# Kernel tuning notes

Measured on AMD Instinct MI355X. Metric: run time of the kernel, lower is better.

## Reference

```python
import jax, jax.numpy as jnp
import numpy as np

D_MODEL = 1024
N_Q = 16
N_KV = 4
HEAD = 64
T = 4096
B = 1


def setup_inputs() -> dict:
    key = jax.random.key(0)
    ks = jax.random.split(key, 5)
    q_dim = N_Q * HEAD
    kv_dim = N_KV * HEAD
    s = 0.02
    return {
        "x": jax.random.normal(ks[0], (B, T, D_MODEL), dtype=jnp.float32),
        "W_q": jax.random.normal(ks[1], (D_MODEL, q_dim), dtype=jnp.float32) * s,
        "W_k": jax.random.normal(ks[2], (D_MODEL, kv_dim), dtype=jnp.float32) * s,
        "W_v": jax.random.normal(ks[3], (D_MODEL, kv_dim), dtype=jnp.float32) * s,
        "W_o": jax.random.normal(ks[4], (q_dim, D_MODEL), dtype=jnp.float32) * s,
    }


def reference(x, W_q, W_k, W_v, W_o):
    Bsz, Tlen, _ = x.shape
    n_q_per_kv = N_Q // N_KV
    scale = jnp.asarray(np.sqrt(HEAD), x.dtype)
    # projections, split heads: (B, T, H*D) -> (B, H, T, D)
    q = (x @ W_q).reshape(Bsz, Tlen, N_Q, HEAD).transpose(0, 2, 1, 3)
    k = (x @ W_k).reshape(Bsz, Tlen, N_KV, HEAD).transpose(0, 2, 1, 3)
    v = (x @ W_v).reshape(Bsz, Tlen, N_KV, HEAD).transpose(0, 2, 1, 3)
    # GQA: duplicate KV heads to match query heads (repeat_interleave on head dim)
    k = jnp.repeat(k, n_q_per_kv, axis=1)
    v = jnp.repeat(v, n_q_per_kv, axis=1)
    attn = jnp.einsum("bhqd,bhkd->bhqk", q, k) / scale  # (B, H, T, T)
    causal = jnp.tril(jnp.ones((Tlen, Tlen), dtype=bool))
    attn = jnp.where(causal[None, None], attn, -jnp.inf)
    attn = jax.nn.softmax(attn, axis=-1)
    out = jnp.einsum("bhqk,bhkd->bhqd", attn, v)  # (B, H, T, D)
    out = out.transpose(0, 2, 1, 3).reshape(Bsz, Tlen, N_Q * HEAD)
    return out @ W_o
```

## Files before the change

### kernel.cpp

```cpp
#include <hip/hip_runtime.h>

typedef __bf16 bf16;
typedef __bf16 bf16x4 __attribute__((ext_vector_type(4)));
typedef __bf16 bf16x8 __attribute__((ext_vector_type(8)));
typedef float  f32x4  __attribute__((ext_vector_type(4)));

#define DEV __device__ __forceinline__

#if __has_builtin(__builtin_amdgcn_exp2f)
#define EXP2(x) __builtin_amdgcn_exp2f(x)
#else
#define EXP2(x) exp2f(x)
#endif

DEV void gload16(const void* g, void* l) {
  __builtin_amdgcn_global_load_lds((const __attribute__((address_space(1))) void*)g,
                                   (__attribute__((address_space(3))) void*)l, 16, 0, 0);
}

DEV f32x4 mfma16(bf16x8 a, bf16x8 b, f32x4 c) {
  return __builtin_amdgcn_mfma_f32_16x16x32_bf16(a, b, c, 0, 0, 0);
}

#define QSCALE 0.18033688011112042f

__global__ __launch_bounds__(256) void cast_x_kernel(const float* __restrict__ x,
                                                     bf16* __restrict__ xb) {
  int i = blockIdx.x * 256 + threadIdx.x;
  f32x4 v = ((const f32x4*)x)[i];
  bf16x4 o = {(bf16)v.x, (bf16)v.y, (bf16)v.z, (bf16)v.w};
  ((bf16x4*)xb)[i] = o;
}

__global__ __launch_bounds__(256) void wtrans_kernel(const float* __restrict__ sQ,
                                                     const float* __restrict__ sK,
                                                     const float* __restrict__ sV,
                                                     bf16* __restrict__ dst) {
  __shared__ float tile[32][33];
  int k0 = blockIdx.x * 32, n0 = blockIdx.y * 32;
  int tx = threadIdx.x & 31, ty = threadIdx.x >> 5;
  const float* src; int ld, nb;
  if (n0 < 1024)      { src = sQ; ld = 1024; nb = 0; }
  else if (n0 < 1280) { src = sK; ld = 256;  nb = 1024; }
  else                { src = sV; ld = 256;  nb = 1280; }
#pragma unroll
  for (int i = 0; i < 4; i++) {
    int r = ty + 8 * i;
    tile[r][tx] = src[(size_t)(k0 + r) * ld + (n0 - nb + tx)];
  }
  __syncthreads();
#pragma unroll
  for (int i = 0; i < 4; i++) {
    int r = ty + 8 * i;
    dst[(size_t)(n0 + r) * 1024 + k0 + tx] = (bf16)tile[tx][r];
  }
}

template <int MODE>
__global__ __launch_bounds__(256) void gemm_kernel(const bf16* __restrict__ A,
                                                   const bf16* __restrict__ B,
                                                   float* __restrict__ Cf,
                                                   bf16* __restrict__ qkbuf,
                                                   bf16* __restrict__ vtbuf, int N) {
  constexpr int K = 1024;
  __shared__ bf16 Al[2][64 * 32];
  __shared__ bf16 Bl[2][128 * 32];
  int tid = threadIdx.x;
  int w = tid >> 6, lane = tid & 63;
  int g = lane >> 4, r15 = lane & 15;
  int wr = w >> 1, wc = w & 1;
  int m0 = blockIdx.y * 64, n0 = blockIdx.x * 128;

  int sra = 16 * w + (lane >> 2);
  int srb = 32 * w + (lane >> 2);
  int ss = lane & 3;
  const bf16* a0 = A + (size_t)(m0 + sra) * K + 8 * (ss ^ ((sra >> 1) & 3));
  const bf16* b0 = B + (size_t)(n0 + srb) * K + 8 * (ss ^ ((srb >> 1) & 3));
  const bf16* b1 = B + (size_t)(n0 + srb + 16) * K + 8 * (ss ^ (((srb + 16) >> 1) & 3));

#define GSTAGE(kk_, b_) do { \
    char* ad = (char*)Al[b_] + w * 1024; \
    char* bd = (char*)Bl[b_] + w * 2048; \
    gload16(a0 + (kk_), ad); \
    gload16(b0 + (kk_), bd); \
    gload16(b1 + (kk_), bd + 1024); \
  } while (0)

  GSTAGE(0, 0);
  __syncthreads();

  f32x4 acc[2][4] = {};
  for (int kk = 0; kk < K; kk += 32) {
    int cur = (kk >> 5) & 1;
    if (kk + 32 < K) GSTAGE(kk + 32, cur ^ 1);
    bf16x8 af[2], bb[4];
#pragma unroll
    for (int i = 0; i < 2; i++) {
      int m = 32 * wr + 16 * i + r15;
      af[i] = *(const bf16x8*)((const char*)Al[cur] + m * 64 + 16 * (g ^ ((m >> 1) & 3)));
    }
#pragma unroll
    for (int i = 0; i < 4; i++) {
      int n = 64 * wc + 16 * i + r15;
      bb[i] = *(const bf16x8*)((const char*)Bl[cur] + n * 64 + 16 * (g ^ ((n >> 1) & 3)));
    }
    __builtin_amdgcn_s_setprio(1);
#pragma unroll
    for (int mi = 0; mi < 2; mi++)
#pragma unroll
      for (int ni = 0; ni < 4; ni++)
        acc[mi][ni] = mfma16(af[mi], bb[ni], acc[mi][ni]);
    __builtin_amdgcn_s_setprio(0);
    __syncthreads();
  }

  if (MODE == 0) {
#pragma unroll
    for (int mi = 0; mi < 2; mi++) {
      int mg = m0 + 32 * wr + 16 * mi + 4 * g;
#pragma unroll
      for (int ni = 0; ni < 4; ni++) {
        int ng = n0 + 64 * wc + 16 * ni + r15;
#pragma unroll
        for (int r = 0; r < 4; r++)
          Cf[(size_t)(mg + r) * N + ng] = acc[mi][ni][r];
      }
    }
  } else {
    if (n0 < 1280) {
      float qs = (n0 < 1024) ? QSCALE : 1.0f;
#pragma unroll
      for (int mi = 0; mi < 2; mi++) {
        int tg = m0 + 32 * wr + 16 * mi + 4 * g;
#pragma unroll
        for (int ni = 0; ni < 4; ni++) {
          int ng = n0 + 64 * wc + 16 * ni + r15;
#pragma unroll
          for (int r = 0; r < 4; r++)
            qkbuf[(size_t)(tg + r) * 1280 + ng] = (bf16)(acc[mi][ni][r] * qs);
        }
      }
    } else {
#pragma unroll
      for (int mi = 0; mi < 2; mi++) {
        int tg = m0 + 32 * wr + 16 * mi + 4 * g;
#pragma unroll
        for (int ni = 0; ni < 4; ni++) {
          int vcol = n0 + 64 * wc + 16 * ni + r15 - 1280;
          bf16x4 pk = {(bf16)acc[mi][ni][0], (bf16)acc[mi][ni][1],
                       (bf16)acc[mi][ni][2], (bf16)acc[mi][ni][3]};
          *(bf16x4*)(vtbuf + (size_t)vcol * 4096 + tg) = pk;
        }
      }
    }
  }
#undef GSTAGE
}

__global__ __launch_bounds__(256) void attn_kernel(const bf16* __restrict__ qk,
                                                   const bf16* __restrict__ vt,
                                                   bf16* __restrict__ out) {
  __shared__ bf16 Kt[2][64 * 64];
  __shared__ bf16 Vt[2][64 * 64];
  __shared__ bf16 Pl[4][16][72];
  int tid = threadIdx.x, w = tid >> 6, lane = tid & 63;
  int g = lane >> 4, r15 = lane & 15;
  int j = blockIdx.x;
  int h = j & 15, tI = 63 - (j >> 4);
  int kh = h >> 2;
  int na = tI + 1;
  int qw = 64 * tI + 16 * w;

  bf16x8 bq[2];
#pragma unroll
  for (int ks = 0; ks < 2; ks++)
    bq[ks] = *(const bf16x8*)(qk + (size_t)(qw + r15) * 1280 + h * 64 + 32 * ks + 8 * g);

  float l_run = 0.f;
  f32x4 oacc[4] = {};

  int sw8 = 8 * ((lane & 7) ^ (lane >> 3));
  const bf16* kbase = qk + 1024 + (size_t)kh * 64 + (size_t)(16 * w + (lane >> 3)) * 1280 + sw8;
  const bf16* vbase = vt + ((size_t)(kh * 64 + 16 * w + (lane >> 3))) * 4096 + sw8;

#define STAGE(t0_, b_) do { \
    char* kd = (char*)Kt[b_] + w * 2048; \
    char* vd = (char*)Vt[b_] + w * 2048; \
    gload16(kbase + (size_t)(t0_) * 1280, kd); \
    gload16(kbase + (size_t)(t0_) * 1280 + (size_t)8 * 1280, kd + 1024); \
    gload16(vbase + (t0_), vd); \
    gload16(vbase + (t0_) + 8 * 4096, vd + 1024); \
  } while (0)

  STAGE(0, 0);
  __syncthreads();

  for (int it = 0; it < na; ++it) {
    int cur = it & 1;
    int t0 = 64 * it;
    if (it + 1 < na) STAGE(64 * (it + 1), cur ^ 1);
    bool need_mask = (it == na - 1);
    const char* Kc = (const char*)Kt[cur];
    const char* Vc = (const char*)Vt[cur];

    f32x4 s[4];
    __builtin_amdgcn_s_setprio(1);
#pragma unroll
    for (int mi = 0; mi < 4; mi++) {
      int kv = 16 * mi + r15;
      bf16x8 k0f = *(const bf16x8*)(Kc + kv * 128 + 16 * (g ^ (kv & 7)));
      bf16x8 k1f = *(const bf16x8*)(Kc + kv * 128 + 16 * ((4 + g) ^ (kv & 7)));
      f32x4 z = {};
      z = mfma16(k0f, bq[0], z);
      z = mfma16(k1f, bq[1], z);
      s[mi] = z;
    }
    __builtin_amdgcn_s_setprio(0);

    int qg = qw + r15;
    float psum = 0.f;
    bf16 pb[16];
#pragma unroll
    for (int mi = 0; mi < 4; mi++)
#pragma unroll
      for (int r = 0; r < 4; r++) {
        float v = s[mi][r];
        if (need_mask) {
          int kvg = t0 + 16 * mi + 4 * g + r;
          v = (kvg > qg) ? -1e30f : v;
        }
        float pp = EXP2(v);
        psum += pp;
        pb[4 * mi + r] = (bf16)pp;
      }
    l_run += psum;

#pragma unroll
    for (int mi = 0; mi < 4; mi++) {
      bf16x4 pk = {pb[4 * mi], pb[4 * mi + 1], pb[4 * mi + 2], pb[4 * mi + 3]};
      *(bf16x4*)((char*)&Pl[w][r15][0] + mi * 32 + g * 8) = pk;
    }
    bf16x8 ap0 = *(const bf16x8*)((const char*)&Pl[w][r15][0] + 16 * g);
    bf16x8 ap1 = *(const bf16x8*)((const char*)&Pl[w][r15][0] + 64 + 16 * g);
    __builtin_amdgcn_s_setprio(1);
#pragma unroll
    for (int ni = 0; ni < 4; ni++) {
      int d = 16 * ni + r15;
      bf16x8 bv0 = *(const bf16x8*)(Vc + d * 128 + 16 * (g ^ (d & 7)));
      bf16x8 bv1 = *(const bf16x8*)(Vc + d * 128 + 16 * ((4 + g) ^ (d & 7)));
      oacc[ni] = mfma16(ap0, bv0, oacc[ni]);
      oacc[ni] = mfma16(ap1, bv1, oacc[ni]);
    }
    __builtin_amdgcn_s_setprio(0);
    __syncthreads();
  }
#undef STAGE

  float lsum = l_run;
  lsum += __shfl_xor(lsum, 16);
  lsum += __shfl_xor(lsum, 32);
  float linv = 1.0f / lsum;
  float li[4];
#pragma unroll
  for (int r = 0; r < 4; r++) li[r] = __shfl(linv, 4 * g + r);
#pragma unroll
  for (int ni = 0; ni < 4; ni++)
#pragma unroll
    for (int r = 0; r < 4; r++)
      out[(size_t)(qw + 4 * g + r) * 1024 + h * 64 + 16 * ni + r15] =
          (bf16)(oacc[ni][r] * li[r]);
}

extern "C" void kernel_launch(void* const* d_in, const int* in_sizes, int n_in,
                              void* d_out, int out_size, void* d_ws, size_t ws_size,
                              hipStream_t stream) {
  const float* x  = (const float*)d_in[0];
  const float* Wq = (const float*)d_in[1];
  const float* Wk = (const float*)d_in[2];
  const float* Wv = (const float*)d_in[3];
  const float* Wo = (const float*)d_in[4];
  float* out = (float*)d_out;
  char* ws = (char*)d_ws;
  bf16* xb    = (bf16*)(ws);
  bf16* wqkvt = (bf16*)(ws + 8388608);
  bf16* wot   = (bf16*)(ws + 11534336);
  bf16* qkbuf = (bf16*)(ws + 13631488);
  bf16* vtb   = (bf16*)(ws + 24117248);

  cast_x_kernel<<<4096, 256, 0, stream>>>(x, xb);
  wtrans_kernel<<<dim3(32, 48), 256, 0, stream>>>(Wq, Wk, Wv, wqkvt);
  wtrans_kernel<<<dim3(32, 32), 256, 0, stream>>>(Wo, Wo, Wo, wot);
  gemm_kernel<1><<<dim3(12, 64), 256, 0, stream>>>(xb, wqkvt, nullptr, qkbuf, vtb, 1536);
  attn_kernel<<<dim3(1024), 256, 0, stream>>>(qkbuf, vtb, xb);
  gemm_kernel<0><<<dim3(8, 64), 256, 0, stream>>>(xb, wot, out, nullptr, nullptr, 1024);
}
```

Measured before the change: 184.5 us.

## Merge prep kernels into one launch and double GEMM K-tile to 64

Combines the x cast and the two weight transpose/cast kernels into a single prep kernel that dispatches on block index, removing two kernel launches. The GEMM now stages 64-wide K slices per iteration instead of 32, with a new 8-way XOR swizzle for 128-byte LDS rows, which halves the number of barriers and loop iterations. The cost is double the LDS footprint per block (48KB instead of 24KB), which may reduce occupancy, and more registers held for fragments.

```diff
diff --git a/kernel.cpp b/kernel.cpp
--- a/kernel.cpp
+++ b/kernel.cpp
@@ -24,25 +24,35 @@
 
 #define QSCALE 0.18033688011112042f
 
-__global__ __launch_bounds__(256) void cast_x_kernel(const float* __restrict__ x,
-                                                     bf16* __restrict__ xb) {
-  int i = blockIdx.x * 256 + threadIdx.x;
-  f32x4 v = ((const f32x4*)x)[i];
-  bf16x4 o = {(bf16)v.x, (bf16)v.y, (bf16)v.z, (bf16)v.w};
-  ((bf16x4*)xb)[i] = o;
-}
-
-__global__ __launch_bounds__(256) void wtrans_kernel(const float* __restrict__ sQ,
-                                                     const float* __restrict__ sK,
-                                                     const float* __restrict__ sV,
-                                                     bf16* __restrict__ dst) {
+__global__ __launch_bounds__(256) void prep_kernel(const float* __restrict__ x,
+                                                   const float* __restrict__ Wq,
+                                                   const float* __restrict__ Wk,
+                                                   const float* __restrict__ Wv,
+                                                   const float* __restrict__ Wo,
+                                                   bf16* __restrict__ xb,
+                                                   bf16* __restrict__ wqkvt,
+                                                   bf16* __restrict__ wot) {
   __shared__ float tile[32][33];
-  int k0 = blockIdx.x * 32, n0 = blockIdx.y * 32;
+  int bid = blockIdx.x;
+  if (bid < 4096) {
+    int i = bid * 256 + threadIdx.x;
+    f32x4 v = ((const f32x4*)x)[i];
+    bf16x4 o = {(bf16)v.x, (bf16)v.y, (bf16)v.z, (bf16)v.w};
+    ((bf16x4*)xb)[i] = o;
+    return;
+  }
+  const float* src; int ld, nb; bf16* dst; int idx;
+  if (bid < 5632) {
+    idx = bid - 4096; dst = wqkvt;
+    int n0 = (idx >> 5) * 32;
+    if (n0 < 1024)      { src = Wq; ld = 1024; nb = 0; }
+    else if (n0 < 1280) { src = Wk; ld = 256;  nb = 1024; }
+    else                { src = Wv; ld = 256;  nb = 1280; }
+  } else {
+    idx = bid - 5632; dst = wot; src = Wo; ld = 1024; nb = 0;
+  }
+  int k0 = (idx & 31) * 32, n0 = (idx >> 5) * 32;
   int tx = threadIdx.x & 31, ty = threadIdx.x >> 5;
-  const float* src; int ld, nb;
-  if (n0 < 1024)      { src = sQ; ld = 1024; nb = 0; }
-  else if (n0 < 1280) { src = sK; ld = 256;  nb = 1024; }
-  else                { src = sV; ld = 256;  nb = 1280; }
 #pragma unroll
   for (int i = 0; i < 4; i++) {
     int r = ty + 8 * i;
@@ -63,53 +73,64 @@
                                                    bf16* __restrict__ qkbuf,
                                                    bf16* __restrict__ vtbuf, int N) {
   constexpr int K = 1024;
-  __shared__ bf16 Al[2][64 * 32];
-  __shared__ bf16 Bl[2][128 * 32];
+  __shared__ bf16 Al[2][64 * 64];
+  __shared__ bf16 Bl[2][128 * 64];
   int tid = threadIdx.x;
   int w = tid >> 6, lane = tid & 63;
   int g = lane >> 4, r15 = lane & 15;
   int wr = w >> 1, wc = w & 1;
   int m0 = blockIdx.y * 64, n0 = blockIdx.x * 128;
 
-  int sra = 16 * w + (lane >> 2);
-  int srb = 32 * w + (lane >> 2);
-  int ss = lane & 3;
-  const bf16* a0 = A + (size_t)(m0 + sra) * K + 8 * (ss ^ ((sra >> 1) & 3));
-  const bf16* b0 = B + (size_t)(n0 + srb) * K + 8 * (ss ^ ((srb >> 1) & 3));
-  const bf16* b1 = B + (size_t)(n0 + srb + 16) * K + 8 * (ss ^ (((srb + 16) >> 1) & 3));
+  int sl = lane & 7;
+  int srw = lane >> 3;
+  const bf16* Abase = A + (size_t)m0 * K;
+  const bf16* Bbase = B + (size_t)n0 * K;
 
 #define GSTAGE(kk_, b_) do { \
-    char* ad = (char*)Al[b_] + w * 1024; \
-    char* bd = (char*)Bl[b_] + w * 2048; \
-    gload16(a0 + (kk_), ad); \
-    gload16(b0 + (kk_), bd); \
-    gload16(b1 + (kk_), bd + 1024); \
+    _Pragma("unroll") \
+    for (int i = 0; i < 2; i++) { \
+      int ra = 16 * w + 8 * i + srw; \
+      gload16(Abase + (size_t)ra * K + (kk_) + 8 * (sl ^ (ra & 7)), \
+              (char*)Al[b_] + (16 * w + 8 * i) * 128); \
+    } \
+    _Pragma("unroll") \
+    for (int i = 0; i < 4; i++) { \
+      int rb = 32 * w + 8 * i + srw; \
+      gload16(Bbase + (size_t)rb * K + (kk_) + 8 * (sl ^ (rb & 7)), \
+              (char*)Bl[b_] + (32 * w + 8 * i) * 128); \
+    } \
   } while (0)
 
   GSTAGE(0, 0);
   __syncthreads();
 
   f32x4 acc[2][4] = {};
-  for (int kk = 0; kk < K; kk += 32) {
-    int cur = (kk >> 5) & 1;
-    if (kk + 32 < K) GSTAGE(kk + 32, cur ^ 1);
-    bf16x8 af[2], bb[4];
-#pragma unroll
-    for (int i = 0; i < 2; i++) {
-      int m = 32 * wr + 16 * i + r15;
-      af[i] = *(const bf16x8*)((const char*)Al[cur] + m * 64 + 16 * (g ^ ((m >> 1) & 3)));
-    }
-#pragma unroll
-    for (int i = 0; i < 4; i++) {
-      int n = 64 * wc + 16 * i + r15;
-      bb[i] = *(const bf16x8*)((const char*)Bl[cur] + n * 64 + 16 * (g ^ ((n >> 1) & 3)));
+  for (int kk = 0; kk < K; kk += 64) {
+    int cur = (kk >> 6) & 1;
+    if (kk + 64 < K) GSTAGE(kk + 64, cur ^ 1);
+    bf16x8 af[2][2], bb[4][2];
+#pragma unroll
+    for (int mi = 0; mi < 2; mi++) {
+      int m = 32 * wr + 16 * mi + r15;
+#pragma unroll
+      for (int ks = 0; ks < 2; ks++)
+        af[mi][ks] = *(const bf16x8*)((const char*)Al[cur] + m * 128 + 16 * ((4 * ks + g) ^ (m & 7)));
+    }
+#pragma unroll
+    for (int ni = 0; ni < 4; ni++) {
+      int n = 64 * wc + 16 * ni + r15;
+#pragma unroll
+      for (int ks = 0; ks < 2; ks++)
+        bb[ni][ks] = *(const bf16x8*)((const char*)Bl[cur] + n * 128 + 16 * ((4 * ks + g) ^ (n & 7)));
     }
     __builtin_amdgcn_s_setprio(1);
 #pragma unroll
-    for (int mi = 0; mi < 2; mi++)
-#pragma unroll
-      for (int ni = 0; ni < 4; ni++)
-        acc[mi][ni] = mfma16(af[mi], bb[ni], acc[mi][ni]);
+    for (int ks = 0; ks < 2; ks++)
+#pragma unroll
+      for (int mi = 0; mi < 2; mi++)
+#pragma unroll
+        for (int ni = 0; ni < 4; ni++)
+          acc[mi][ni] = mfma16(af[mi][ks], bb[ni][ks], acc[mi][ni]);
     __builtin_amdgcn_s_setprio(0);
     __syncthreads();
   }
@@ -287,9 +308,7 @@
   bf16* qkbuf = (bf16*)(ws + 13631488);
   bf16* vtb   = (bf16*)(ws + 24117248);
 
-  cast_x_kernel<<<4096, 256, 0, stream>>>(x, xb);
-  wtrans_kernel<<<dim3(32, 48), 256, 0, stream>>>(Wq, Wk, Wv, wqkvt);
-  wtrans_kernel<<<dim3(32, 32), 256, 0, stream>>>(Wo, Wo, Wo, wot);
+  prep_kernel<<<6656, 256, 0, stream>>>(x, Wq, Wk, Wv, Wo, xb, wqkvt, wot);
   gemm_kernel<1><<<dim3(12, 64), 256, 0, stream>>>(xb, wqkvt, nullptr, qkbuf, vtb, 1536);
   attn_kernel<<<dim3(1024), 256, 0, stream>>>(qkbuf, vtb, xb);
   gemm_kernel<0><<<dim3(8, 64), 256, 0, stream>>>(xb, wot, out, nullptr, nullptr, 1024);
```

Result: faster. 173.4 us (-6.0%).
